# Performance work log

Hardware: AMD Instinct MI355X
Metric: run time of the kernel (lower is better)

## Reference

```python
import jax, jax.numpy as jnp
import numpy as np

E = 1_000_000      # number of edges
T = 2_000_000      # number of angle triplets
EDGE_DIM = 64
HIDDEN = 128
LN_EPS = 1e-5


def _layer_norm(x, gamma, beta):
    mu = jnp.mean(x, axis=-1, keepdims=True)
    var = jnp.mean(jnp.square(x - mu), axis=-1, keepdims=True)
    return (x - mu) * jax.lax.rsqrt(var + LN_EPS) * gamma + beta


def setup_inputs() -> dict:
    key = jax.random.key(0)
    ks = jax.random.split(key, 8)
    in_dim = 2 * EDGE_DIM + 4  # 132

    def lin(k, fan_in, fan_out):
        bound = 1.0 / np.sqrt(fan_in)
        kw, kb = jax.random.split(k)
        W = jax.random.uniform(kw, (fan_in, fan_out), jnp.float32, -bound, bound)
        b = jax.random.uniform(kb, (fan_out,), jnp.float32, -bound, bound)
        return W, b

    W1, b1 = lin(ks[0], in_dim, HIDDEN)
    W2, b2 = lin(ks[1], HIDDEN, HIDDEN)
    W3, b3 = lin(ks[2], HIDDEN, EDGE_DIM)

    return {
        "edge_feat": jax.random.normal(ks[3], (E, EDGE_DIM), jnp.float32),
        "triplet_idx": jax.random.randint(ks[4], (T, 2), 0, E, jnp.int64) if jax.config.jax_enable_x64 else jax.random.randint(ks[4], (T, 2), 0, E, jnp.int32),
        "triplet_geo": jax.random.uniform(ks[5], (T, 4), jnp.float32),
        "W1": W1, "b1": b1,
        "g1": jnp.ones((HIDDEN,), jnp.float32), "be1": jnp.zeros((HIDDEN,), jnp.float32),
        "W2": W2, "b2": b2,
        "g2": jnp.ones((HIDDEN,), jnp.float32), "be2": jnp.zeros((HIDDEN,), jnp.float32),
        "W3": W3, "b3": b3,
        "gn": jnp.ones((EDGE_DIM,), jnp.float32), "bn": jnp.zeros((EDGE_DIM,), jnp.float32),
    }


def reference(edge_feat, triplet_idx, triplet_geo,
              W1, b1, g1, be1, W2, b2, g2, be2, W3, b3, gn, bn):
    num_edges = edge_feat.shape[0]
    e_ij = triplet_idx[:, 0]
    e_kj = triplet_idx[:, 1]

    f_ij = edge_feat[e_ij]                      # [T, edge_dim] gather
    f_kj = edge_feat[e_kj]                      # [T, edge_dim] gather
    x = jnp.concatenate([f_ij, f_kj, triplet_geo], axis=1)  # [T, 2*edge_dim+4]

    # mlp_phi: Linear -> SiLU -> LayerNorm -> Linear -> SiLU -> LayerNorm
    h = _layer_norm(jax.nn.silu(x @ W1 + b1), g1, be1)
    m = _layer_norm(jax.nn.silu(h @ W2 + b2), g2, be2)  # [T, hidden]

    # scatter-mean over e_ij with dim_size = num_edges
    sums = jax.ops.segment_sum(m, e_ij, num_segments=num_edges)
    cnts = jax.ops.segment_sum(jnp.ones((m.shape[0],), m.dtype), e_ij, num_segments=num_edges)
    agg = sums / jnp.maximum(cnts, 1.0)[:, None]         # [E, hidden]

    out = edge_feat + (agg @ W3 + b3)
    return _layer_norm(out, gn, bn)
```

## Files before the change

kernel.cpp:

```cpp
#include <hip/hip_runtime.h>
#include <hip/hip_bf16.h>
#include <stdint.h>

typedef __attribute__((ext_vector_type(8))) short short8;
typedef __attribute__((ext_vector_type(4))) float f32x4;
typedef unsigned short u16;

#define N_E 1000000
#define N_T 2000000
#define NB_SCAN 3907
#define NWG_TRIP 31250

#define OFF_MBUF 0ULL
#define OFF_EBF  256000000ULL
#define OFF_CUR  384000000ULL
#define OFF_WT1  388000000ULL
#define OFF_WT2  (OFF_WT1 + 40960ULL)
#define OFF_WT3  (OFF_WT2 + 32768ULL)
#define OFF_S2   (OFF_WT3 + 16384ULL)
#define OFF_C2   (OFF_S2 + 512ULL)
#define OFF_S3   (OFF_C2 + 512ULL)
#define OFF_T3   (OFF_S3 + 256ULL)

#define DO_HIST    0ULL
#define DO_SORTEDT 4000000ULL
#define DO_BSUM    12000000ULL

#define LDS_HM   0
#define LDS_P1S  16384
#define LDS_P1Q  16896
#define LDS_P2S  17408
#define LDS_P2Q  17920
#define LDS_TOTAL 18432

__device__ __forceinline__ u16 f2bf(float f) {
  union { float f; uint32_t u; } c; c.f = f;
  uint32_t u = c.u;
  return (u16)((u + 0x7FFFu + ((u >> 16) & 1u)) >> 16);
}
__device__ __forceinline__ uint32_t pkbf(float lo, float hi) {
  float2 t; t.x = lo; t.y = hi;
  __hip_bfloat162 h = __float22bfloat162_rn(t);
  uint32_t u; __builtin_memcpy(&u, &h, 4);
  return u;
}
__device__ __forceinline__ float blo(uint32_t u) {
  union { uint32_t u; float f; } c; c.u = u << 16; return c.f;
}
__device__ __forceinline__ float bhi(uint32_t u) {
  union { uint32_t u; float f; } c; c.u = u & 0xffff0000u; return c.f;
}
__device__ __forceinline__ float silu(float y) {
  return y * __builtin_amdgcn_rcpf(1.0f + __expf(-y));
}

#define MFMA16(a, b, c) __builtin_amdgcn_mfma_f32_16x16x32_bf16((a), (b), (c), 0, 0, 0)


__global__ __launch_bounds__(256) void k_conv_edge(const float* __restrict__ ef,
                                                   u16* __restrict__ ebf) {
  int i = blockIdx.x * 256 + threadIdx.x;
  float4 v = ((const float4*)ef)[i];
  ushort4 o;
  o.x = f2bf(v.x); o.y = f2bf(v.y); o.z = f2bf(v.z); o.w = f2bf(v.w);
  ((ushort4*)ebf)[i] = o;
}

__global__ __launch_bounds__(256) void k_pack_w(const float* __restrict__ W1,
                                                const float* __restrict__ W2,
                                                const float* __restrict__ W3,
                                                const float* __restrict__ g1,
                                                const float* __restrict__ g2,
                                                u16* __restrict__ wt1,
                                                u16* __restrict__ wt2,
                                                u16* __restrict__ wt3) {
  int i = blockIdx.x * 256 + threadIdx.x;
  if (i < 20480) {
    int n = i / 160, k = i - n * 160;
    wt1[i] = (k < 132) ? f2bf(W1[k * 128 + n]) : (u16)0;
  } else if (i < 36864) {
    int i2 = i - 20480;
    int n = i2 >> 7, k = i2 & 127;
    wt2[i2] = f2bf(g1[k] * W2[k * 128 + n]);
  } else if (i < 45056) {
    int i3 = i - 36864;
    int n = i3 >> 7, k = i3 & 127;
    wt3[i3] = f2bf(g2[k] * W3[k * 64 + n]);
  }
}

__global__ __launch_bounds__(256) void k_pack_vec(
    const float* __restrict__ W2, const float* __restrict__ W3,
    const float* __restrict__ g1, const float* __restrict__ be1, const float* __restrict__ b2,
    const float* __restrict__ g2, const float* __restrict__ be2,
    float* __restrict__ s2, float* __restrict__ c2,
    float* __restrict__ s3, float* __restrict__ t3) {
  int t = threadIdx.x;
  if (t < 128) {
    float a = 0.f, b = 0.f;
    for (int k = 0; k < 128; ++k) {
      float w = W2[k * 128 + t];
      a += g1[k] * w; b += be1[k] * w;
    }
    s2[t] = a; c2[t] = b + b2[t];
  } else if (t < 192) {
    int n = t - 128;
    float a = 0.f, b = 0.f;
    for (int k = 0; k < 128; ++k) {
      float w = W3[k * 64 + n];
      a += g2[k] * w; b += be2[k] * w;
    }
    s3[n] = a; t3[n] = b;
  }
}


__global__ __launch_bounds__(256) void k_hist(const int2* __restrict__ tidx,
                                              int* __restrict__ hist) {
  int t = blockIdx.x * 256 + threadIdx.x;
  if (t < N_T) atomicAdd(&hist[tidx[t].x], 1);
}

__global__ __launch_bounds__(256) void k_scan_bsum(const int* __restrict__ hist,
                                                   int* __restrict__ bsum) {
  int b = blockIdx.x, tid = threadIdx.x;
  int i = b * 256 + tid;
  int v = (i < N_E) ? hist[i] : 0;
#pragma unroll
  for (int d = 1; d < 64; d <<= 1) v += __shfl_xor(v, d);
  __shared__ int ws4[4];
  if ((tid & 63) == 0) ws4[tid >> 6] = v;
  __syncthreads();
  if (tid == 0) bsum[b] = ws4[0] + ws4[1] + ws4[2] + ws4[3];
}

__global__ __launch_bounds__(256) void k_scan_boffs(int* __restrict__ bsum, int nb) {
  __shared__ int ws4[4];
  __shared__ int carry;
  int tid = threadIdx.x, lane = tid & 63, w = tid >> 6;
  if (tid == 0) carry = 0;
  __syncthreads();
  for (int base = 0; base < nb; base += 256) {
    int i = base + tid;
    int v = (i < nb) ? bsum[i] : 0;
    int inc = v;
#pragma unroll
    for (int d = 1; d < 64; d <<= 1) { int u = __shfl_up(inc, d); if (lane >= d) inc += u; }
    if (lane == 63) ws4[w] = inc;
    __syncthreads();
    int off = 0;
    for (int k = 0; k < w; ++k) off += ws4[k];
    int excl = carry + off + inc - v;
    int total = ws4[0] + ws4[1] + ws4[2] + ws4[3];
    __syncthreads();
    if (i < nb) bsum[i] = excl;
    if (tid == 0) carry += total;
    __syncthreads();
  }
}

__global__ __launch_bounds__(256) void k_scan_fin(const int* __restrict__ hist,
                                                  const int* __restrict__ bsum,
                                                  int* __restrict__ cursor) {
  int b = blockIdx.x, tid = threadIdx.x, lane = tid & 63, w = tid >> 6;
  int i = b * 256 + tid;
  int v = (i < N_E) ? hist[i] : 0;
  int inc = v;
#pragma unroll
  for (int d = 1; d < 64; d <<= 1) { int u = __shfl_up(inc, d); if (lane >= d) inc += u; }
  __shared__ int ws4[4];
  if (lane == 63) ws4[w] = inc;
  __syncthreads();
  int off = 0;
  for (int k = 0; k < w; ++k) off += ws4[k];
  if (i < N_E) cursor[i] = bsum[b] + off + inc - v;
}

__global__ __launch_bounds__(256) void k_scatter(const int2* __restrict__ tidx,
                                                 int* __restrict__ cursor,
                                                 int* __restrict__ sortedT) {
  int t = blockIdx.x * 256 + threadIdx.x;
  if (t < N_T) {
    int pos = atomicAdd(&cursor[tidx[t].x], 1);
    sortedT[pos] = t;
  }
}


__global__ __launch_bounds__(256, 5) void k_triplet(
    const u16* __restrict__ ebf, const int2* __restrict__ tidx,
    const float4* __restrict__ geo4, const int* __restrict__ sortedT,
    const u16* __restrict__ wt1, const u16* __restrict__ wt2, const u16* __restrict__ wt3,
    const float* __restrict__ b1,
    const float* __restrict__ s2v, const float* __restrict__ c2v,
    const float* __restrict__ s3v,
    u16* __restrict__ mbuf) {
  __shared__ __align__(16) char smem[LDS_TOTAL];
  float* P1S = (float*)(smem + LDS_P1S);
  float* P1Q = (float*)(smem + LDS_P1Q);
  float* P2S = (float*)(smem + LDS_P2S);
  float* P2Q = (float*)(smem + LDS_P2Q);

  const int tid = threadIdx.x;
  const int wave = tid >> 6, lane = tid & 63;
  const int wm = wave >> 1, wn = wave & 1;
  const int l15 = lane & 15, lg = lane >> 4;

  const int q = NWG_TRIP >> 3, r = NWG_TRIP & 7;
  int orig = blockIdx.x;
  int xcd = orig & 7, idx = orig >> 3;
  int bid = (xcd < r ? xcd * (q + 1) : r * (q + 1) + (xcd - r) * q) + idx;
  const int i0 = bid * 64;

  const int tA = wn * 32 + l15;
  const int tB = tA + 16;
  int stA = sortedT[i0 + tA];
  int stB = sortedT[i0 + tB];
  int2 pA = tidx[stA];
  int2 pB = tidx[stB];

  const short8* eb = (const short8*)ebf;
  short8 bxA0 = eb[(size_t)pA.x * 8 + lg];
  short8 bxA1 = eb[(size_t)pA.x * 8 + 4 + lg];
  short8 bxA2 = eb[(size_t)pA.y * 8 + lg];
  short8 bxA3 = eb[(size_t)pA.y * 8 + 4 + lg];
  short8 bxB0 = eb[(size_t)pB.x * 8 + lg];
  short8 bxB1 = eb[(size_t)pB.x * 8 + 4 + lg];
  short8 bxB2 = eb[(size_t)pB.y * 8 + lg];
  short8 bxB3 = eb[(size_t)pB.y * 8 + 4 + lg];

  short8 btA = (short8)0, btB = (short8)0;
  if (lg == 0) {
    float4 ga = geo4[stA];
    btA[0] = (short)f2bf(ga.x); btA[1] = (short)f2bf(ga.y);
    btA[2] = (short)f2bf(ga.z); btA[3] = (short)f2bf(ga.w);
    float4 gb = geo4[stB];
    btB[0] = (short)f2bf(gb.x); btB[1] = (short)f2bf(gb.y);
    btB[2] = (short)f2bf(gb.z); btB[3] = (short)f2bf(gb.w);
  }

  f32x4 acc[4][2];
#pragma unroll
  for (int mf = 0; mf < 4; ++mf) { acc[mf][0] = (f32x4)0.f; acc[mf][1] = (f32x4)0.f; }
  const short8* w1p = (const short8*)wt1;
#pragma unroll
  for (int s5 = 0; s5 < 5; ++s5) {
    short8 b0, b1x;
    if (s5 == 0) { b0 = bxA0; b1x = bxB0; }
    else if (s5 == 1) { b0 = bxA1; b1x = bxB1; }
    else if (s5 == 2) { b0 = bxA2; b1x = bxB2; }
    else if (s5 == 3) { b0 = bxA3; b1x = bxB3; }
    else { b0 = btA; b1x = btB; }
#pragma unroll
    for (int mf = 0; mf < 4; ++mf) {
      short8 aw = w1p[(wm * 64 + mf * 16 + l15) * 20 + s5 * 4 + lg];
      acc[mf][0] = MFMA16(aw, b0, acc[mf][0]);
      acc[mf][1] = MFMA16(aw, b1x, acc[mf][1]);
    }
  }

  {
    float4 b1f[4];
#pragma unroll
    for (int mf = 0; mf < 4; ++mf)
      b1f[mf] = *(const float4*)(b1 + wm * 64 + mf * 16 + lg * 4);
    float st[2] = {0.f, 0.f}, sq[2] = {0.f, 0.f};
#pragma unroll
    for (int mf = 0; mf < 4; ++mf)
#pragma unroll
      for (int f = 0; f < 2; ++f)
#pragma unroll
        for (int q2 = 0; q2 < 4; ++q2) {
          float v = silu(acc[mf][f][q2] + b1f[mf][q2]);
          acc[mf][f][q2] = v;
          st[f] += v; sq[f] += v * v;
        }
#pragma unroll
    for (int f = 0; f < 2; ++f) {
      st[f] += __shfl_xor(st[f], 16); sq[f] += __shfl_xor(sq[f], 16);
      st[f] += __shfl_xor(st[f], 32); sq[f] += __shfl_xor(sq[f], 32);
    }
    if (lg == 0) {
#pragma unroll
      for (int f = 0; f < 2; ++f) {
        int trip = wn * 32 + f * 16 + l15;
        P1S[trip * 2 + wm] = st[f];
        P1Q[trip * 2 + wm] = sq[f];
      }
    }
#pragma unroll
    for (int mf = 0; mf < 4; ++mf)
#pragma unroll
      for (int f = 0; f < 2; ++f) {
        int trip = wn * 32 + f * 16 + l15;
        uint2 w;
        w.x = pkbf(acc[mf][f][0], acc[mf][f][1]);
        w.y = pkbf(acc[mf][f][2], acc[mf][f][3]);
        *(uint2*)(smem + LDS_HM + trip * 256 +
                  ((wm * 128 + mf * 32 + lg * 8) ^ ((trip & 7) << 4))) = w;
      }
  }
  __syncthreads();

#pragma unroll
  for (int mf = 0; mf < 4; ++mf) { acc[mf][0] = (f32x4)0.f; acc[mf][1] = (f32x4)0.f; }
  const short8* w2p = (const short8*)wt2;
#pragma unroll
  for (int s4 = 0; s4 < 4; ++s4) {
    short8 bx0, bx1;
    {
      int trip = wn * 32 + l15;
      bx0 = *(const short8*)(smem + LDS_HM + trip * 256 +
                             ((s4 * 64 + lg * 16) ^ ((trip & 7) << 4)));
      int trip2 = trip + 16;
      bx1 = *(const short8*)(smem + LDS_HM + trip2 * 256 +
                             ((s4 * 64 + lg * 16) ^ ((trip2 & 7) << 4)));
    }
#pragma unroll
    for (int mf = 0; mf < 4; ++mf) {
      short8 aw = w2p[(wm * 64 + mf * 16 + l15) * 16 + s4 * 4 + lg];
      acc[mf][0] = MFMA16(aw, bx0, acc[mf][0]);
      acc[mf][1] = MFMA16(aw, bx1, acc[mf][1]);
    }
  }

  {
    float4 s2f[4], c2f[4];
#pragma unroll
    for (int mf = 0; mf < 4; ++mf) {
      s2f[mf] = *(const float4*)(s2v + wm * 64 + mf * 16 + lg * 4);
      c2f[mf] = *(const float4*)(c2v + wm * 64 + mf * 16 + lg * 4);
    }
    float mu[2], inv[2];
#pragma unroll
    for (int f = 0; f < 2; ++f) {
      int trip = wn * 32 + f * 16 + l15;
      float sm = P1S[trip * 2] + P1S[trip * 2 + 1];
      float qq = P1Q[trip * 2] + P1Q[trip * 2 + 1];
      mu[f] = sm * 0.0078125f;
      inv[f] = rsqrtf(fmaxf(qq * 0.0078125f - mu[f] * mu[f], 0.f) + 1e-5f);
    }
    float st[2] = {0.f, 0.f}, sq[2] = {0.f, 0.f};
#pragma unroll
    for (int mf = 0; mf < 4; ++mf)
#pragma unroll
      for (int f = 0; f < 2; ++f)
#pragma unroll
        for (int q2 = 0; q2 < 4; ++q2) {
          float y = inv[f] * (acc[mf][f][q2] - mu[f] * s2f[mf][q2]) + c2f[mf][q2];
          float v = silu(y);
          acc[mf][f][q2] = v;
          st[f] += v; sq[f] += v * v;
        }
#pragma unroll
    for (int f = 0; f < 2; ++f) {
      st[f] += __shfl_xor(st[f], 16); sq[f] += __shfl_xor(sq[f], 16);
      st[f] += __shfl_xor(st[f], 32); sq[f] += __shfl_xor(sq[f], 32);
    }
    if (lg == 0) {
#pragma unroll
      for (int f = 0; f < 2; ++f) {
        int trip = wn * 32 + f * 16 + l15;
        P2S[trip * 2 + wm] = st[f];
        P2Q[trip * 2 + wm] = sq[f];
      }
    }
  }
  __syncthreads();

#pragma unroll
  for (int mf = 0; mf < 4; ++mf)
#pragma unroll
    for (int f = 0; f < 2; ++f) {
      int trip = wn * 32 + f * 16 + l15;
      uint2 w;
      w.x = pkbf(acc[mf][f][0], acc[mf][f][1]);
      w.y = pkbf(acc[mf][f][2], acc[mf][f][3]);
      *(uint2*)(smem + LDS_HM + trip * 256 +
                ((wm * 128 + mf * 32 + lg * 8) ^ ((trip & 7) << 4))) = w;
    }
  __syncthreads();

  f32x4 acc3[2][2];
#pragma unroll
  for (int mf = 0; mf < 2; ++mf) { acc3[mf][0] = (f32x4)0.f; acc3[mf][1] = (f32x4)0.f; }
  const short8* w3p = (const short8*)wt3;
#pragma unroll
  for (int s4 = 0; s4 < 4; ++s4) {
    short8 bx0, bx1;
    {
      int trip = wn * 32 + l15;
      bx0 = *(const short8*)(smem + LDS_HM + trip * 256 +
                             ((s4 * 64 + lg * 16) ^ ((trip & 7) << 4)));
      int trip2 = trip + 16;
      bx1 = *(const short8*)(smem + LDS_HM + trip2 * 256 +
                             ((s4 * 64 + lg * 16) ^ ((trip2 & 7) << 4)));
    }
#pragma unroll
    for (int mf = 0; mf < 2; ++mf) {
      short8 aw = w3p[(wm * 32 + mf * 16 + l15) * 16 + s4 * 4 + lg];
      acc3[mf][0] = MFMA16(aw, bx0, acc3[mf][0]);
      acc3[mf][1] = MFMA16(aw, bx1, acc3[mf][1]);
    }
  }

  {
    float4 s3f[2];
#pragma unroll
    for (int mf = 0; mf < 2; ++mf)
      s3f[mf] = *(const float4*)(s3v + wm * 32 + mf * 16 + lg * 4);
#pragma unroll
    for (int f = 0; f < 2; ++f) {
      int trip = wn * 32 + f * 16 + l15;
      float sm = P2S[trip * 2] + P2S[trip * 2 + 1];
      float qq = P2Q[trip * 2] + P2Q[trip * 2 + 1];
      float mu3 = sm * 0.0078125f;
      float inv3 = rsqrtf(fmaxf(qq * 0.0078125f - mu3 * mu3, 0.f) + 1e-5f);
      u16* rowp = mbuf + (size_t)(i0 + trip) * 64;
#pragma unroll
      for (int mf = 0; mf < 2; ++mf) {
        float y0 = inv3 * (acc3[mf][f][0] - mu3 * s3f[mf][0]);
        float y1 = inv3 * (acc3[mf][f][1] - mu3 * s3f[mf][1]);
        float y2 = inv3 * (acc3[mf][f][2] - mu3 * s3f[mf][2]);
        float y3 = inv3 * (acc3[mf][f][3] - mu3 * s3f[mf][3]);
        uint64_t wv = (uint64_t)pkbf(y0, y1) | ((uint64_t)pkbf(y2, y3) << 32);
        __builtin_nontemporal_store(wv, (uint64_t*)(rowp + wm * 32 + mf * 16 + lg * 4));
      }
    }
  }
}


__global__ __launch_bounds__(256) void k_final(
    const u16* __restrict__ mbuf, const int* __restrict__ cursor,
    const float* __restrict__ ef, const float* __restrict__ b3,
    const float* __restrict__ t3, const float* __restrict__ gn,
    const float* __restrict__ bn, float* __restrict__ out) {
  int g = blockIdx.x * 256 + threadIdx.x;
  int e = g >> 2, s = g & 3;
  int end = cursor[e];
  int start = (e > 0) ? cursor[e - 1] : 0;
  int c = end - start;
  float ic = 1.0f / (float)((c > 0) ? c : 1);
  float tw = (c > 0) ? 1.0f : 0.0f;
  float a[16];
#pragma unroll
  for (int i = 0; i < 16; ++i) a[i] = 0.f;
  for (int r = start; r < end; ++r) {
    const uint4* mp = (const uint4*)(mbuf + (size_t)r * 64 + s * 16);
    uint4 u0 = mp[0], u1 = mp[1];
    a[0] += blo(u0.x); a[1] += bhi(u0.x); a[2] += blo(u0.y); a[3] += bhi(u0.y);
    a[4] += blo(u0.z); a[5] += bhi(u0.z); a[6] += blo(u0.w); a[7] += bhi(u0.w);
    a[8] += blo(u1.x); a[9] += bhi(u1.x); a[10] += blo(u1.y); a[11] += bhi(u1.y);
    a[12] += blo(u1.z); a[13] += bhi(u1.z); a[14] += blo(u1.w); a[15] += bhi(u1.w);
  }
  float x[16];
  const float4* fe = (const float4*)(ef + (size_t)e * 64 + s * 16);
  const float4* p3 = (const float4*)(b3 + s * 16);
  const float4* pt = (const float4*)(t3 + s * 16);
#pragma unroll
  for (int i = 0; i < 4; ++i) {
    float4 b = fe[i], cc = p3[i], d = pt[i];
    x[4 * i + 0] = b.x + a[4 * i + 0] * ic + cc.x + tw * d.x;
    x[4 * i + 1] = b.y + a[4 * i + 1] * ic + cc.y + tw * d.y;
    x[4 * i + 2] = b.z + a[4 * i + 2] * ic + cc.z + tw * d.z;
    x[4 * i + 3] = b.w + a[4 * i + 3] * ic + cc.w + tw * d.w;
  }
  float sum = 0.f, ss = 0.f;
#pragma unroll
  for (int i = 0; i < 16; ++i) { sum += x[i]; ss += x[i] * x[i]; }
  sum += __shfl_xor(sum, 1); ss += __shfl_xor(ss, 1);
  sum += __shfl_xor(sum, 2); ss += __shfl_xor(ss, 2);
  float mu = sum * (1.0f / 64.0f);
  float inv = rsqrtf(ss * (1.0f / 64.0f) - mu * mu + 1e-5f);
  float4* po = (float4*)(out + (size_t)e * 64 + s * 16);
#pragma unroll
  for (int i = 0; i < 4; ++i) {
    float4 gv = ((const float4*)(gn + s * 16))[i];
    float4 bv = ((const float4*)(bn + s * 16))[i];
    float4 o;
    o.x = (x[4 * i + 0] - mu) * inv * gv.x + bv.x;
    o.y = (x[4 * i + 1] - mu) * inv * gv.y + bv.y;
    o.z = (x[4 * i + 2] - mu) * inv * gv.z + bv.z;
    o.w = (x[4 * i + 3] - mu) * inv * gv.w + bv.w;
    po[i] = o;
  }
}

extern "C" void kernel_launch(void* const* d_in, const int* in_sizes, int n_in,
                              void* d_out, int out_size, void* d_ws, size_t ws_size,
                              hipStream_t stream) {
  const float* edge_feat = (const float*)d_in[0];
  const int2* tidx = (const int2*)d_in[1];
  const float4* geo4 = (const float4*)d_in[2];
  const float* W1 = (const float*)d_in[3];
  const float* b1 = (const float*)d_in[4];
  const float* g1 = (const float*)d_in[5];
  const float* be1 = (const float*)d_in[6];
  const float* W2 = (const float*)d_in[7];
  const float* b2 = (const float*)d_in[8];
  const float* g2 = (const float*)d_in[9];
  const float* be2 = (const float*)d_in[10];
  const float* W3 = (const float*)d_in[11];
  const float* b3 = (const float*)d_in[12];
  const float* gn = (const float*)d_in[13];
  const float* bn = (const float*)d_in[14];

  char* ws = (char*)d_ws;
  u16* mbuf = (u16*)(ws + OFF_MBUF);
  u16* ebf = (u16*)(ws + OFF_EBF);
  int* cursor = (int*)(ws + OFF_CUR);
  u16* wt1 = (u16*)(ws + OFF_WT1);
  u16* wt2 = (u16*)(ws + OFF_WT2);
  u16* wt3 = (u16*)(ws + OFF_WT3);
  float* s2 = (float*)(ws + OFF_S2);
  float* c2 = (float*)(ws + OFF_C2);
  float* s3 = (float*)(ws + OFF_S3);
  float* t3 = (float*)(ws + OFF_T3);

  char* ob = (char*)d_out;
  int* hist = (int*)(ob + DO_HIST);
  int* sortedT = (int*)(ob + DO_SORTEDT);
  int* bsum = (int*)(ob + DO_BSUM);
  float* out = (float*)d_out;

  hipMemsetAsync(hist, 0, (size_t)N_E * 4, stream);
  k_conv_edge<<<62500, 256, 0, stream>>>(edge_feat, ebf);
  k_pack_w<<<176, 256, 0, stream>>>(W1, W2, W3, g1, g2, wt1, wt2, wt3);
  k_pack_vec<<<1, 256, 0, stream>>>(W2, W3, g1, be1, b2, g2, be2, s2, c2, s3, t3);

  k_hist<<<7813, 256, 0, stream>>>(tidx, hist);
  k_scan_bsum<<<NB_SCAN, 256, 0, stream>>>(hist, bsum);
  k_scan_boffs<<<1, 256, 0, stream>>>(bsum, NB_SCAN);
  k_scan_fin<<<NB_SCAN, 256, 0, stream>>>(hist, bsum, cursor);
  k_scatter<<<7813, 256, 0, stream>>>(tidx, cursor, sortedT);

  k_triplet<<<NWG_TRIP, 256, 0, stream>>>(ebf, tidx, geo4, sortedT,
                                          wt1, wt2, wt3, b1, s2, c2, s3, mbuf);
  k_final<<<15625, 256, 0, stream>>>(mbuf, cursor, edge_feat, b3, t3, gn, bn, out);
}
```

Baseline: 1.200 ms.

## Make triplet kernel persistent with software-prefetched gathers across tiles

The triplet MLP kernel now launches 768 persistent workgroups, each walking a contiguous chunk of 41 tiles instead of one workgroup per tile. Inside the loop the next tile's sortedT/tidx indices and bf16 edge-feature gathers are issued after the first GEMM so gather latency overlaps compute, and the per-tile bias/LN vectors are hoisted out of the loop. Occupancy hint drops from 5 to 3 waves to make room for the extra live registers. The output store becomes a regular rather than nontemporal store, and the XCD-aware block remapping is dropped, which may reduce L2 locality for sorted neighbours.

```diff
diff --git a/kernel.cpp b/kernel.cpp
--- a/kernel.cpp
+++ b/kernel.cpp
@@ -9,7 +9,9 @@
 #define N_E 1000000
 #define N_T 2000000
 #define NB_SCAN 3907
-#define NWG_TRIP 31250
+#define TILES 31250
+#define GRID_TRIP 768
+#define CHUNK 41
 
 #define OFF_MBUF 0ULL
 #define OFF_EBF  256000000ULL
@@ -187,7 +189,7 @@
 }
 
 
-__global__ __launch_bounds__(256, 5) void k_triplet(
+__global__ __launch_bounds__(256, 3) void k_triplet(
     const u16* __restrict__ ebf, const int2* __restrict__ tidx,
     const float4* __restrict__ geo4, const int* __restrict__ sortedT,
     const u16* __restrict__ wt1, const u16* __restrict__ wt2, const u16* __restrict__ wt3,
@@ -206,29 +208,40 @@
   const int wm = wave >> 1, wn = wave & 1;
   const int l15 = lane & 15, lg = lane >> 4;
 
-  const int q = NWG_TRIP >> 3, r = NWG_TRIP & 7;
-  int orig = blockIdx.x;
-  int xcd = orig & 7, idx = orig >> 3;
-  int bid = (xcd < r ? xcd * (q + 1) : r * (q + 1) + (xcd - r) * q) + idx;
-  const int i0 = bid * 64;
+  const int t0 = blockIdx.x * CHUNK;
+  if (t0 >= TILES) return;
+  const int t1 = (t0 + CHUNK < TILES) ? (t0 + CHUNK) : TILES;
 
   const int tA = wn * 32 + l15;
   const int tB = tA + 16;
-  int stA = sortedT[i0 + tA];
-  int stB = sortedT[i0 + tB];
-  int2 pA = tidx[stA];
-  int2 pB = tidx[stB];
-
   const short8* eb = (const short8*)ebf;
-  short8 bxA0 = eb[(size_t)pA.x * 8 + lg];
-  short8 bxA1 = eb[(size_t)pA.x * 8 + 4 + lg];
-  short8 bxA2 = eb[(size_t)pA.y * 8 + lg];
-  short8 bxA3 = eb[(size_t)pA.y * 8 + 4 + lg];
-  short8 bxB0 = eb[(size_t)pB.x * 8 + lg];
-  short8 bxB1 = eb[(size_t)pB.x * 8 + 4 + lg];
-  short8 bxB2 = eb[(size_t)pB.y * 8 + lg];
-  short8 bxB3 = eb[(size_t)pB.y * 8 + 4 + lg];
-
+  const short8* w1p = (const short8*)wt1;
+  const short8* w2p = (const short8*)wt2;
+  const short8* w3p = (const short8*)wt3;
+
+  float4 b1f[4], s2f[4], c2f[4];
+#pragma unroll
+  for (int mf = 0; mf < 4; ++mf) {
+    b1f[mf] = *(const float4*)(b1 + wm * 64 + mf * 16 + lg * 4);
+    s2f[mf] = *(const float4*)(s2v + wm * 64 + mf * 16 + lg * 4);
+    c2f[mf] = *(const float4*)(c2v + wm * 64 + mf * 16 + lg * 4);
+  }
+  float4 s3f[2];
+#pragma unroll
+  for (int mf = 0; mf < 2; ++mf)
+    s3f[mf] = *(const float4*)(s3v + wm * 32 + mf * 16 + lg * 4);
+
+  int stA = sortedT[t0 * 64 + tA];
+  int stB = sortedT[t0 * 64 + tB];
+  int2 pA = tidx[stA], pB = tidx[stB];
+  short8 g0 = eb[(size_t)pA.x * 8 + lg];
+  short8 g1r = eb[(size_t)pA.x * 8 + 4 + lg];
+  short8 g2r = eb[(size_t)pA.y * 8 + lg];
+  short8 g3 = eb[(size_t)pA.y * 8 + 4 + lg];
+  short8 g4 = eb[(size_t)pB.x * 8 + lg];
+  short8 g5 = eb[(size_t)pB.x * 8 + 4 + lg];
+  short8 g6 = eb[(size_t)pB.y * 8 + lg];
+  short8 g7 = eb[(size_t)pB.y * 8 + 4 + lg];
   short8 btA = (short8)0, btB = (short8)0;
   if (lg == 0) {
     float4 ga = geo4[stA];
@@ -239,55 +252,150 @@
     btB[2] = (short)f2bf(gb.z); btB[3] = (short)f2bf(gb.w);
   }
 
-  f32x4 acc[4][2];
-#pragma unroll
-  for (int mf = 0; mf < 4; ++mf) { acc[mf][0] = (f32x4)0.f; acc[mf][1] = (f32x4)0.f; }
-  const short8* w1p = (const short8*)wt1;
-#pragma unroll
-  for (int s5 = 0; s5 < 5; ++s5) {
-    short8 b0, b1x;
-    if (s5 == 0) { b0 = bxA0; b1x = bxB0; }
-    else if (s5 == 1) { b0 = bxA1; b1x = bxB1; }
-    else if (s5 == 2) { b0 = bxA2; b1x = bxB2; }
-    else if (s5 == 3) { b0 = bxA3; b1x = bxB3; }
-    else { b0 = btA; b1x = btB; }
-#pragma unroll
-    for (int mf = 0; mf < 4; ++mf) {
-      short8 aw = w1p[(wm * 64 + mf * 16 + l15) * 20 + s5 * 4 + lg];
-      acc[mf][0] = MFMA16(aw, b0, acc[mf][0]);
-      acc[mf][1] = MFMA16(aw, b1x, acc[mf][1]);
-    }
-  }
-
-  {
-    float4 b1f[4];
-#pragma unroll
-    for (int mf = 0; mf < 4; ++mf)
-      b1f[mf] = *(const float4*)(b1 + wm * 64 + mf * 16 + lg * 4);
-    float st[2] = {0.f, 0.f}, sq[2] = {0.f, 0.f};
-#pragma unroll
-    for (int mf = 0; mf < 4; ++mf)
-#pragma unroll
-      for (int f = 0; f < 2; ++f)
-#pragma unroll
-        for (int q2 = 0; q2 < 4; ++q2) {
-          float v = silu(acc[mf][f][q2] + b1f[mf][q2]);
-          acc[mf][f][q2] = v;
-          st[f] += v; sq[f] += v * v;
+  for (int t = t0; t < t1; ++t) {
+    const int tn = (t + 1 < t1) ? (t + 1) : t0;
+    int stA_n = sortedT[tn * 64 + tA];
+    int stB_n = sortedT[tn * 64 + tB];
+    int2 pA_n = tidx[stA_n];
+    int2 pB_n = tidx[stB_n];
+
+    __syncthreads();
+
+    f32x4 acc[4][2];
+#pragma unroll
+    for (int mf = 0; mf < 4; ++mf) { acc[mf][0] = (f32x4)0.f; acc[mf][1] = (f32x4)0.f; }
+#pragma unroll
+    for (int s5 = 0; s5 < 5; ++s5) {
+      short8 b0, b1x;
+      if (s5 == 0) { b0 = g0; b1x = g4; }
+      else if (s5 == 1) { b0 = g1r; b1x = g5; }
+      else if (s5 == 2) { b0 = g2r; b1x = g6; }
+      else if (s5 == 3) { b0 = g3; b1x = g7; }
+      else { b0 = btA; b1x = btB; }
+#pragma unroll
+      for (int mf = 0; mf < 4; ++mf) {
+        short8 aw = w1p[(wm * 64 + mf * 16 + l15) * 20 + s5 * 4 + lg];
+        acc[mf][0] = MFMA16(aw, b0, acc[mf][0]);
+        acc[mf][1] = MFMA16(aw, b1x, acc[mf][1]);
+      }
+    }
+
+    short8 n0 = eb[(size_t)pA_n.x * 8 + lg];
+    short8 n1 = eb[(size_t)pA_n.x * 8 + 4 + lg];
+    short8 n2 = eb[(size_t)pA_n.y * 8 + lg];
+    short8 n3 = eb[(size_t)pA_n.y * 8 + 4 + lg];
+    short8 n4 = eb[(size_t)pB_n.x * 8 + lg];
+    short8 n5 = eb[(size_t)pB_n.x * 8 + 4 + lg];
+    short8 n6 = eb[(size_t)pB_n.y * 8 + lg];
+    short8 n7 = eb[(size_t)pB_n.y * 8 + 4 + lg];
+    short8 nbtA = (short8)0, nbtB = (short8)0;
+    if (lg == 0) {
+      float4 ga = geo4[stA_n];
+      nbtA[0] = (short)f2bf(ga.x); nbtA[1] = (short)f2bf(ga.y);
+      nbtA[2] = (short)f2bf(ga.z); nbtA[3] = (short)f2bf(ga.w);
+      float4 gb = geo4[stB_n];
+      nbtB[0] = (short)f2bf(gb.x); nbtB[1] = (short)f2bf(gb.y);
+      nbtB[2] = (short)f2bf(gb.z); nbtB[3] = (short)f2bf(gb.w);
+    }
+
+    {
+      float st[2] = {0.f, 0.f}, sq[2] = {0.f, 0.f};
+#pragma unroll
+      for (int mf = 0; mf < 4; ++mf)
+#pragma unroll
+        for (int f = 0; f < 2; ++f)
+#pragma unroll
+          for (int q2 = 0; q2 < 4; ++q2) {
+            float v = silu(acc[mf][f][q2] + b1f[mf][q2]);
+            acc[mf][f][q2] = v;
+            st[f] += v; sq[f] += v * v;
+          }
+#pragma unroll
+      for (int f = 0; f < 2; ++f) {
+        st[f] += __shfl_xor(st[f], 16); sq[f] += __shfl_xor(sq[f], 16);
+        st[f] += __shfl_xor(st[f], 32); sq[f] += __shfl_xor(sq[f], 32);
+      }
+      if (lg == 0) {
+#pragma unroll
+        for (int f = 0; f < 2; ++f) {
+          int trip = wn * 32 + f * 16 + l15;
+          P1S[trip * 2 + wm] = st[f];
+          P1Q[trip * 2 + wm] = sq[f];
         }
-#pragma unroll
-    for (int f = 0; f < 2; ++f) {
-      st[f] += __shfl_xor(st[f], 16); sq[f] += __shfl_xor(sq[f], 16);
-      st[f] += __shfl_xor(st[f], 32); sq[f] += __shfl_xor(sq[f], 32);
-    }
-    if (lg == 0) {
+      }
+#pragma unroll
+      for (int mf = 0; mf < 4; ++mf)
+#pragma unroll
+        for (int f = 0; f < 2; ++f) {
+          int trip = wn * 32 + f * 16 + l15;
+          uint2 w;
+          w.x = pkbf(acc[mf][f][0], acc[mf][f][1]);
+          w.y = pkbf(acc[mf][f][2], acc[mf][f][3]);
+          *(uint2*)(smem + LDS_HM + trip * 256 +
+                    ((wm * 128 + mf * 32 + lg * 8) ^ ((trip & 7) << 4))) = w;
+        }
+    }
+    __syncthreads();
+
+#pragma unroll
+    for (int mf = 0; mf < 4; ++mf) { acc[mf][0] = (f32x4)0.f; acc[mf][1] = (f32x4)0.f; }
+#pragma unroll
+    for (int s4 = 0; s4 < 4; ++s4) {
+      short8 bx0, bx1;
+      {
+        int trip = wn * 32 + l15;
+        bx0 = *(const short8*)(smem + LDS_HM + trip * 256 +
+                               ((s4 * 64 + lg * 16) ^ ((trip & 7) << 4)));
+        int trip2 = trip + 16;
+        bx1 = *(const short8*)(smem + LDS_HM + trip2 * 256 +
+                               ((s4 * 64 + lg * 16) ^ ((trip2 & 7) << 4)));
+      }
+#pragma unroll
+      for (int mf = 0; mf < 4; ++mf) {
+        short8 aw = w2p[(wm * 64 + mf * 16 + l15) * 16 + s4 * 4 + lg];
+        acc[mf][0] = MFMA16(aw, bx0, acc[mf][0]);
+        acc[mf][1] = MFMA16(aw, bx1, acc[mf][1]);
+      }
+    }
+
+    {
+      float mu[2], inv[2];
 #pragma unroll
       for (int f = 0; f < 2; ++f) {
         int trip = wn * 32 + f * 16 + l15;
-        P1S[trip * 2 + wm] = st[f];
-        P1Q[trip * 2 + wm] = sq[f];
-      }
-    }
+        float sm = P1S[trip * 2] + P1S[trip * 2 + 1];
+        float qq = P1Q[trip * 2] + P1Q[trip * 2 + 1];
+        mu[f] = sm * 0.0078125f;
+        inv[f] = rsqrtf(fmaxf(qq * 0.0078125f - mu[f] * mu[f], 0.f) + 1e-5f);
+      }
+      float st[2] = {0.f, 0.f}, sq[2] = {0.f, 0.f};
+#pragma unroll
+      for (int mf = 0; mf < 4; ++mf)
+#pragma unroll
+        for (int f = 0; f < 2; ++f)
+#pragma unroll
+          for (int q2 = 0; q2 < 4; ++q2) {
+            float y = inv[f] * (acc[mf][f][q2] - mu[f] * s2f[mf][q2]) + c2f[mf][q2];
+            float v = silu(y);
+            acc[mf][f][q2] = v;
+            st[f] += v; sq[f] += v * v;
+          }
+#pragma unroll
+      for (int f = 0; f < 2; ++f) {
+        st[f] += __shfl_xor(st[f], 16); sq[f] += __shfl_xor(sq[f], 16);
+        st[f] += __shfl_xor(st[f], 32); sq[f] += __shfl_xor(sq[f], 32);
+      }
+      if (lg == 0) {
+#pragma unroll
+        for (int f = 0; f < 2; ++f) {
+          int trip = wn * 32 + f * 16 + l15;
+          P2S[trip * 2 + wm] = st[f];
+          P2Q[trip * 2 + wm] = sq[f];
+        }
+      }
+    }
+    __syncthreads();
+
 #pragma unroll
     for (int mf = 0; mf < 4; ++mf)
 #pragma unroll
@@ -299,134 +407,58 @@
         *(uint2*)(smem + LDS_HM + trip * 256 +
                   ((wm * 128 + mf * 32 + lg * 8) ^ ((trip & 7) << 4))) = w;
       }
-  }
-  __syncthreads();
-
-#pragma unroll
-  for (int mf = 0; mf < 4; ++mf) { acc[mf][0] = (f32x4)0.f; acc[mf][1] = (f32x4)0.f; }
-  const short8* w2p = (const short8*)wt2;
-#pragma unroll
-  for (int s4 = 0; s4 < 4; ++s4) {
-    short8 bx0, bx1;
+    __syncthreads();
+
+    f32x4 acc3[2][2];
+#pragma unroll
+    for (int mf = 0; mf < 2; ++mf) { acc3[mf][0] = (f32x4)0.f; acc3[mf][1] = (f32x4)0.f; }
+#pragma unroll
+    for (int s4 = 0; s4 < 4; ++s4) {
+      short8 bx0, bx1;
+      {
+        int trip = wn * 32 + l15;
+        bx0 = *(const short8*)(smem + LDS_HM + trip * 256 +
+                               ((s4 * 64 + lg * 16) ^ ((trip & 7) << 4)));
+        int trip2 = trip + 16;
+        bx1 = *(const short8*)(smem + LDS_HM + trip2 * 256 +
+                               ((s4 * 64 + lg * 16) ^ ((trip2 & 7) << 4)));
+      }
+#pragma unroll
+      for (int mf = 0; mf < 2; ++mf) {
+        short8 aw = w3p[(wm * 32 + mf * 16 + l15) * 16 + s4 * 4 + lg];
+        acc3[mf][0] = MFMA16(aw, bx0, acc3[mf][0]);
+        acc3[mf][1] = MFMA16(aw, bx1, acc3[mf][1]);
+      }
+    }
+
     {
-      int trip = wn * 32 + l15;
-      bx0 = *(const short8*)(smem + LDS_HM + trip * 256 +
-                             ((s4 * 64 + lg * 16) ^ ((trip & 7) << 4)));
-      int trip2 = trip + 16;
-      bx1 = *(const short8*)(smem + LDS_HM + trip2 * 256 +
-                             ((s4 * 64 + lg * 16) ^ ((trip2 & 7) << 4)));
-    }
-#pragma unroll
-    for (int mf = 0; mf < 4; ++mf) {
-      short8 aw = w2p[(wm * 64 + mf * 16 + l15) * 16 + s4 * 4 + lg];
-      acc[mf][0] = MFMA16(aw, bx0, acc[mf][0]);
-      acc[mf][1] = MFMA16(aw, bx1, acc[mf][1]);
-    }
-  }
-
-  {
-    float4 s2f[4], c2f[4];
-#pragma unroll
-    for (int mf = 0; mf < 4; ++mf) {
-      s2f[mf] = *(const float4*)(s2v + wm * 64 + mf * 16 + lg * 4);
-      c2f[mf] = *(const float4*)(c2v + wm * 64 + mf * 16 + lg * 4);
-    }
-    float mu[2], inv[2];
-#pragma unroll
-    for (int f = 0; f < 2; ++f) {
-      int trip = wn * 32 + f * 16 + l15;
-      float sm = P1S[trip * 2] + P1S[trip * 2 + 1];
-      float qq = P1Q[trip * 2] + P1Q[trip * 2 + 1];
-      mu[f] = sm * 0.0078125f;
-      inv[f] = rsqrtf(fmaxf(qq * 0.0078125f - mu[f] * mu[f], 0.f) + 1e-5f);
-    }
-    float st[2] = {0.f, 0.f}, sq[2] = {0.f, 0.f};
-#pragma unroll
-    for (int mf = 0; mf < 4; ++mf)
-#pragma unroll
-      for (int f = 0; f < 2; ++f)
-#pragma unroll
-        for (int q2 = 0; q2 < 4; ++q2) {
-          float y = inv[f] * (acc[mf][f][q2] - mu[f] * s2f[mf][q2]) + c2f[mf][q2];
-          float v = silu(y);
-          acc[mf][f][q2] = v;
-          st[f] += v; sq[f] += v * v;
-        }
-#pragma unroll
-    for (int f = 0; f < 2; ++f) {
-      st[f] += __shfl_xor(st[f], 16); sq[f] += __shfl_xor(sq[f], 16);
-      st[f] += __shfl_xor(st[f], 32); sq[f] += __shfl_xor(sq[f], 32);
-    }
-    if (lg == 0) {
+      const int i0 = t * 64;
 #pragma unroll
       for (int f = 0; f < 2; ++f) {
         int trip = wn * 32 + f * 16 + l15;
-        P2S[trip * 2 + wm] = st[f];
-        P2Q[trip * 2 + wm] = sq[f];
-      }
-    }
-  }
-  __syncthreads();
-
-#pragma unroll
-  for (int mf = 0; mf < 4; ++mf)
-#pragma unroll
-    for (int f = 0; f < 2; ++f) {
-      int trip = wn * 32 + f * 16 + l15;
-      uint2 w;
-      w.x = pkbf(acc[mf][f][0], acc[mf][f][1]);
-      w.y = pkbf(acc[mf][f][2], acc[mf][f][3]);
-      *(uint2*)(smem + LDS_HM + trip * 256 +
-                ((wm * 128 + mf * 32 + lg * 8) ^ ((trip & 7) << 4))) = w;
-    }
-  __syncthreads();
-
-  f32x4 acc3[2][2];
-#pragma unroll
-  for (int mf = 0; mf < 2; ++mf) { acc3[mf][0] = (f32x4)0.f; acc3[mf][1] = (f32x4)0.f; }
-  const short8* w3p = (const short8*)wt3;
-#pragma unroll
-  for (int s4 = 0; s4 < 4; ++s4) {
-    short8 bx0, bx1;
-    {
-      int trip = wn * 32 + l15;
-      bx0 = *(const short8*)(smem + LDS_HM + trip * 256 +
-                             ((s4 * 64 + lg * 16) ^ ((trip & 7) << 4)));
-      int trip2 = trip + 16;
-      bx1 = *(const short8*)(smem + LDS_HM + trip2 * 256 +
-                             ((s4 * 64 + lg * 16) ^ ((trip2 & 7) << 4)));
-    }
-#pragma unroll
-    for (int mf = 0; mf < 2; ++mf) {
-      short8 aw = w3p[(wm * 32 + mf * 16 + l15) * 16 + s4 * 4 + lg];
-      acc3[mf][0] = MFMA16(aw, bx0, acc3[mf][0]);
-      acc3[mf][1] = MFMA16(aw, bx1, acc3[mf][1]);
-    }
-  }
-
-  {
-    float4 s3f[2];
-#pragma unroll
-    for (int mf = 0; mf < 2; ++mf)
-      s3f[mf] = *(const float4*)(s3v + wm * 32 + mf * 16 + lg * 4);
-#pragma unroll
-    for (int f = 0; f < 2; ++f) {
-      int trip = wn * 32 + f * 16 + l15;
-      float sm = P2S[trip * 2] + P2S[trip * 2 + 1];
-      float qq = P2Q[trip * 2] + P2Q[trip * 2 + 1];
-      float mu3 = sm * 0.0078125f;
-      float inv3 = rsqrtf(fmaxf(qq * 0.0078125f - mu3 * mu3, 0.f) + 1e-5f);
-      u16* rowp = mbuf + (size_t)(i0 + trip) * 64;
-#pragma unroll
-      for (int mf = 0; mf < 2; ++mf) {
-        float y0 = inv3 * (acc3[mf][f][0] - mu3 * s3f[mf][0]);
-        float y1 = inv3 * (acc3[mf][f][1] - mu3 * s3f[mf][1]);
-        float y2 = inv3 * (acc3[mf][f][2] - mu3 * s3f[mf][2]);
-        float y3 = inv3 * (acc3[mf][f][3] - mu3 * s3f[mf][3]);
-        uint64_t wv = (uint64_t)pkbf(y0, y1) | ((uint64_t)pkbf(y2, y3) << 32);
-        __builtin_nontemporal_store(wv, (uint64_t*)(rowp + wm * 32 + mf * 16 + lg * 4));
-      }
-    }
+        float sm = P2S[trip * 2] + P2S[trip * 2 + 1];
+        float qq = P2Q[trip * 2] + P2Q[trip * 2 + 1];
+        float mu3 = sm * 0.0078125f;
+        float inv3 = rsqrtf(fmaxf(qq * 0.0078125f - mu3 * mu3, 0.f) + 1e-5f);
+        u16* rowp = mbuf + (size_t)(i0 + trip) * 64;
+#pragma unroll
+        for (int mf = 0; mf < 2; ++mf) {
+          float y0 = inv3 * (acc3[mf][f][0] - mu3 * s3f[mf][0]);
+          float y1 = inv3 * (acc3[mf][f][1] - mu3 * s3f[mf][1]);
+          float y2 = inv3 * (acc3[mf][f][2] - mu3 * s3f[mf][2]);
+          float y3 = inv3 * (acc3[mf][f][3] - mu3 * s3f[mf][3]);
+          uint2 w;
+          w.x = pkbf(y0, y1);
+          w.y = pkbf(y2, y3);
+          *(uint2*)(rowp + wm * 32 + mf * 16 + lg * 4) = w;
+        }
+      }
+    }
+
+    g0 = n0; g1r = n1; g2r = n2; g3 = n3;
+    g4 = n4; g5 = n5; g6 = n6; g7 = n7;
+    btA = nbtA; btB = nbtB;
+    stA = stA_n; stB = stB_n;
   }
 }
 
@@ -535,7 +567,7 @@
   k_scan_fin<<<NB_SCAN, 256, 0, stream>>>(hist, bsum, cursor);
   k_scatter<<<7813, 256, 0, stream>>>(tidx, cursor, sortedT);
 
-  k_triplet<<<NWG_TRIP, 256, 0, stream>>>(ebf, tidx, geo4, sortedT,
-                                          wt1, wt2, wt3, b1, s2, c2, s3, mbuf);
+  k_triplet<<<GRID_TRIP, 256, 0, stream>>>(ebf, tidx, geo4, sortedT,
+                                           wt1, wt2, wt3, b1, s2, c2, s3, mbuf);
   k_final<<<15625, 256, 0, stream>>>(mbuf, cursor, edge_feat, b3, t3, gn, bn, out);
 }
```

Measured after the change: 1.940 ms. +61.7%, slower.
